# Optimization experiments

Measured on AMD Instinct MI355X. Metric: run time of the kernel, lower is better.

The kernel has to match this reference:

```python
import math
import jax, jax.numpy as jnp
import numpy as np

IN_CH = 512
OUT_CH = 512
KERNEL = 3
STYLE_DIM = 512
B, H, W = 16, 64, 64


def setup_inputs() -> dict:
    key = jax.random.key(0)
    k1, k2, k3, k4 = jax.random.split(key, 4)
    x = jax.random.normal(k1, (B, IN_CH, H, W), dtype=jnp.float32)
    style = jax.random.normal(k2, (B, STYLE_DIM), dtype=jnp.float32)
    # learned params
    weight = jax.random.normal(k3, (1, OUT_CH, IN_CH, KERNEL, KERNEL), dtype=jnp.float32)
    mod_w = jax.random.normal(k4, (IN_CH, STYLE_DIM), dtype=jnp.float32)  # EqualLinear weight (lr_mul=1)
    mod_b = jnp.zeros((IN_CH,), dtype=jnp.float32)
    return {"x": x, "style": style, "weight": weight, "mod_w": mod_w, "mod_b": mod_b}


def reference(x, style, weight, mod_w, mod_b):
    b, c, h, w = x.shape
    lin_scale = 1.0 / math.sqrt(STYLE_DIM)          # EqualLinear scale (lr_mul=1)
    conv_scale = 1.0 / math.sqrt(IN_CH * KERNEL ** 2)
    pad = KERNEL // 2

    # style modulation: (B, in_ch)
    s = style @ (mod_w * lin_scale).T + mod_b
    # modulated per-sample weights: (B, out, in, k, k)
    wmod = conv_scale * weight * s[:, None, :, None, None]
    # demodulation
    d = jax.lax.rsqrt(jnp.sum(wmod ** 2, axis=(2, 3, 4)) + 1e-8)  # (B, out)
    wmod = wmod * d[:, :, None, None, None]

    # grouped conv trick: groups = B
    w_g = wmod.reshape(b * OUT_CH, c, KERNEL, KERNEL)
    x_g = x.reshape(1, b * c, h, w)
    out = jax.lax.conv_general_dilated(
        x_g, w_g,
        window_strides=(1, 1),
        padding=[(pad, pad), (pad, pad)],
        dimension_numbers=("NCHW", "OIHW", "NCHW"),
        feature_group_count=b,
    )
    return out.reshape(b, OUT_CH, out.shape[2], out.shape[3])
```

## Files before the change

### kernel.cpp

```cpp
#include <hip/hip_runtime.h>
#include <hip/hip_bf16.h>
#include <math.h>

typedef __attribute__((ext_vector_type(8))) short short8;
typedef __attribute__((ext_vector_type(4))) float f32x4;

#define BATCH 16
#define IC 512
#define OC 512
#define HW 64
#define SD 512

#define LIN_SCALE 0.04419417382415922f
#define CONV_SCALE 0.014731391274719742f
#define CS2 (1.0f / 4608.0f)

__global__ void k_style(const float* __restrict__ style, const float* __restrict__ mod_w,
                        const float* __restrict__ mod_b, float* __restrict__ s) {
    int idx = blockIdx.x * blockDim.x + threadIdx.x;
    if (idx >= BATCH * IC) return;
    int b = idx / IC, c = idx % IC;
    const float4* st = (const float4*)(style + (size_t)b * SD);
    const float4* mw = (const float4*)(mod_w + (size_t)c * SD);
    float acc = 0.f;
#pragma unroll 4
    for (int k = 0; k < SD / 4; ++k) {
        float4 a = st[k], w = mw[k];
        acc += a.x * w.x + a.y * w.y + a.z * w.z + a.w * w.w;
    }
    s[idx] = acc * LIN_SCALE + mod_b[c];
}

__global__ void k_wsq(const float* __restrict__ weight, float* __restrict__ wsq) {
    int idx = blockIdx.x * blockDim.x + threadIdx.x;
    if (idx >= OC * IC) return;
    const float* w = weight + (size_t)idx * 9;
    float acc = 0.f;
#pragma unroll
    for (int k = 0; k < 9; ++k) { float v = w[k]; acc += v * v; }
    wsq[idx] = acc;
}

__global__ void k_demod(const float* __restrict__ s, const float* __restrict__ wsq,
                        float* __restrict__ dmod) {
    int idx = blockIdx.x * blockDim.x + threadIdx.x;
    if (idx >= BATCH * OC) return;
    int b = idx / OC, o = idx % OC;
    const float* sb = s + (size_t)b * IC;
    const float* wo = wsq + (size_t)o * IC;
    float acc = 0.f;
#pragma unroll 4
    for (int c = 0; c < IC; ++c) { float sv = sb[c]; acc = fmaf(sv * sv, wo[c], acc); }
    dmod[idx] = rsqrtf(acc * CS2 + 1e-8f);
}

__global__ __launch_bounds__(256) void k_wmod(
    const float* __restrict__ weight, const float* __restrict__ s,
    const float* __restrict__ dmod, __hip_bfloat16* __restrict__ wmod) {
    __shared__ float wrow[IC * 9];
    int oc = blockIdx.x, b = blockIdx.y;
    const float* wp = weight + (size_t)oc * IC * 9;
    for (int i = threadIdx.x; i < IC * 9; i += 256) wrow[i] = wp[i];
    __syncthreads();
    float dd = CONV_SCALE * dmod[b * OC + oc];
    const float* sb = s + (size_t)b * IC;
#pragma unroll
    for (int tap = 0; tap < 9; ++tap) {
        int icp = threadIdx.x;
        int ic0 = icp * 2;
        float v0 = wrow[ic0 * 9 + tap] * (sb[ic0] * dd);
        float v1 = wrow[(ic0 + 1) * 9 + tap] * (sb[ic0 + 1] * dd);
        __hip_bfloat162 p;
        p.x = __float2bfloat16(v0);
        p.y = __float2bfloat16(v1);
        *(__hip_bfloat162*)(wmod + ((((size_t)b * 9 + tap) * OC + oc) * IC + ic0)) = p;
    }
}

__global__ __launch_bounds__(512, 2) void k_conv_mfma(
    const float* __restrict__ x, const __hip_bfloat16* __restrict__ wmod,
    float* __restrict__ out) {
    __shared__ short xs[4 * 10 * 66 * 8];

    const int bid = blockIdx.x;
    const int g = bid & 63, sp = bid >> 6;
    const int b = g >> 2, ocg = g & 3;
    const int ocb = ocg * 128, y0 = sp * 8;

    const int t = threadIdx.x;
    const int lane = t & 63, wid = t >> 6;
    const int og = wid >> 2, rg = wid & 3;
    const int l15 = lane & 15, l4 = lane >> 4;

    f32x4 acc[4][8];
#pragma unroll
    for (int m = 0; m < 4; ++m)
#pragma unroll
        for (int n = 0; n < 8; ++n) acc[m][n] = (f32x4){0.f, 0.f, 0.f, 0.f};

    const float* xb = x + (size_t)b * IC * HW * HW;
    const __hip_bfloat16* wb = wmod + (size_t)b * 9 * OC * IC;

    for (int icb = 0; icb < IC; icb += 32) {
        __syncthreads();
        for (int i = t; i < 2640; i += 512) {
            int ichi = i / 660;
            int rem = i - ichi * 660;
            int row = rem / 66;
            int col = rem - row * 66;
            int gy = y0 + row - 1, gx = col - 1;
            float v[8];
            if ((unsigned)gy < 64u && (unsigned)gx < 64u) {
                const float* xp = xb + ((size_t)(icb + ichi * 8) * 64 + gy) * 64 + gx;
#pragma unroll
                for (int j = 0; j < 8; ++j) v[j] = xp[(size_t)j * 4096];
            } else {
#pragma unroll
                for (int j = 0; j < 8; ++j) v[j] = 0.f;
            }
            short8 pk;
#pragma unroll
            for (int j = 0; j < 8; ++j) {
                __hip_bfloat16 bh = __float2bfloat16(v[j]);
                pk[j] = *reinterpret_cast<short*>(&bh);
            }
            *(short8*)&xs[i * 8] = pk;
        }
        __syncthreads();

#pragma unroll
        for (int kw = 0; kw < 3; ++kw) {
            short8 A[3][4];
#pragma unroll
            for (int kh = 0; kh < 3; ++kh)
#pragma unroll
                for (int mt = 0; mt < 4; ++mt) {
                    int oc = ocb + og * 64 + mt * 16 + l15;
                    int tap = kh * 3 + kw;
                    A[kh][mt] = *(const short8*)(wb + (((size_t)tap * OC + oc) * IC + icb + l4 * 8));
                }
#pragma unroll
            for (int cg = 0; cg < 4; ++cg) {
                short8 Bf[4];
#pragma unroll
                for (int ir = 0; ir < 4; ++ir) {
                    int row = rg * 2 + ir;
                    int col = cg * 16 + l15 + kw;
                    Bf[ir] = *(const short8*)&xs[(((l4 * 10 + row) * 66 + col)) * 8];
                }
#pragma unroll
                for (int kh = 0; kh < 3; ++kh)
#pragma unroll
                    for (int mt = 0; mt < 4; ++mt)
#pragma unroll
                        for (int r = 0; r < 2; ++r)
                            acc[mt][r * 4 + cg] = __builtin_amdgcn_mfma_f32_16x16x32_bf16(
                                A[kh][mt], Bf[r + kh], acc[mt][r * 4 + cg], 0, 0, 0);
            }
        }
    }

#pragma unroll
    for (int mt = 0; mt < 4; ++mt)
#pragma unroll
        for (int r = 0; r < 2; ++r)
#pragma unroll
            for (int cg = 0; cg < 4; ++cg) {
                f32x4 v = acc[mt][r * 4 + cg];
                int y = y0 + rg * 2 + r;
                int xcol = cg * 16 + l15;
#pragma unroll
                for (int q = 0; q < 4; ++q) {
                    int oc = ocb + og * 64 + mt * 16 + l4 * 4 + q;
                    out[(((size_t)b * OC + oc) * HW + y) * HW + xcol] = v[q];
                }
            }
}

#define OC_TILE 16
#define ROWS 4
#define ICCH 8
#define XW 67

__global__ __launch_bounds__(256) void k_conv_f32(
    const float* __restrict__ x, const float* __restrict__ weight,
    const float* __restrict__ s, const float* __restrict__ dmod,
    float* __restrict__ out) {
    __shared__ float x_lds[ICCH][ROWS + 2][XW];
    __shared__ float w_lds[OC_TILE][ICCH][9];

    const int b = blockIdx.z;
    const int ocb = blockIdx.y * OC_TILE;
    const int y0 = blockIdx.x * ROWS;

    const int t = threadIdx.x;
    const int gg = t & 63;
    const int ocg = t >> 6;
    const int row = gg >> 4;
    const int col = (gg & 15) * 4;

    float acc[4][4];
#pragma unroll
    for (int j = 0; j < 4; ++j)
#pragma unroll
        for (int i = 0; i < 4; ++i) acc[j][i] = 0.f;

    const float* xb = x + (size_t)b * IC * HW * HW;
    const float* sb = s + (size_t)b * IC;
    const float* db = dmod + (size_t)b * OC;

    for (int icb = 0; icb < IC; icb += ICCH) {
        for (int i = t; i < ICCH * 6 * 66; i += 256) {
            int ic = i / (6 * 66);
            int rem = i - ic * (6 * 66);
            int r = rem / 66;
            int cx = rem - r * 66;
            int gy = y0 + r - 1;
            int gx = cx - 1;
            float v = 0.f;
            if ((unsigned)gy < 64u && (unsigned)gx < 64u)
                v = xb[((size_t)(icb + ic) * 64 + gy) * 64 + gx];
            x_lds[ic][r][cx] = v;
        }
        for (int i = t; i < OC_TILE * ICCH * 9; i += 256) {
            int oc = i / (ICCH * 9);
            int rem = i - oc * (ICCH * 9);
            int ic = rem / 9;
            int kk = rem - ic * 9;
            float sc = CONV_SCALE * sb[icb + ic] * db[ocb + oc];
            w_lds[oc][ic][kk] = weight[((size_t)(ocb + oc) * IC + (icb + ic)) * 9 + kk] * sc;
        }
        __syncthreads();
#pragma unroll
        for (int ic = 0; ic < ICCH; ++ic)
#pragma unroll
            for (int kh = 0; kh < 3; ++kh) {
                float xv[6];
#pragma unroll
                for (int u = 0; u < 6; ++u) xv[u] = x_lds[ic][row + kh][col + u];
#pragma unroll
                for (int kw = 0; kw < 3; ++kw)
#pragma unroll
                    for (int j = 0; j < 4; ++j) {
                        float wv = w_lds[ocg * 4 + j][ic][kh * 3 + kw];
#pragma unroll
                        for (int i2 = 0; i2 < 4; ++i2)
                            acc[j][i2] = fmaf(wv, xv[i2 + kw], acc[j][i2]);
                    }
            }
        __syncthreads();
    }
#pragma unroll
    for (int j = 0; j < 4; ++j) {
        int oc = ocb + ocg * 4 + j;
        float4 v = make_float4(acc[j][0], acc[j][1], acc[j][2], acc[j][3]);
        *(float4*)(out + (((size_t)b * OC + oc) * HW + (y0 + row)) * HW + col) = v;
    }
}

extern "C" void kernel_launch(void* const* d_in, const int* in_sizes, int n_in,
                              void* d_out, int out_size, void* d_ws, size_t ws_size,
                              hipStream_t stream) {
    const float* x      = (const float*)d_in[0];
    const float* style  = (const float*)d_in[1];
    const float* weight = (const float*)d_in[2];
    const float* mod_w  = (const float*)d_in[3];
    const float* mod_b  = (const float*)d_in[4];
    float* out = (float*)d_out;

    float* s    = (float*)d_ws;
    float* wsq  = s + BATCH * IC;
    float* dmod = wsq + (size_t)OC * IC;
    __hip_bfloat16* wmod = (__hip_bfloat16*)(dmod + BATCH * OC);

    const size_t need = (size_t)(BATCH * IC + OC * IC + BATCH * OC) * 4 +
                        (size_t)BATCH * 9 * OC * IC * 2;

    k_style<<<(BATCH * IC + 255) / 256, 256, 0, stream>>>(style, mod_w, mod_b, s);
    k_wsq<<<(OC * IC + 255) / 256, 256, 0, stream>>>(weight, wsq);
    k_demod<<<(BATCH * OC + 255) / 256, 256, 0, stream>>>(s, wsq, dmod);

    if (ws_size >= need) {
        dim3 wg(OC, BATCH);
        k_wmod<<<wg, 256, 0, stream>>>(weight, s, dmod, wmod);
        k_conv_mfma<<<512, 512, 0, stream>>>(x, wmod, out);
    } else {
        dim3 grid(HW / ROWS, OC / OC_TILE, BATCH);
        k_conv_f32<<<grid, 256, 0, stream>>>(x, weight, s, dmod, out);
    }
}
```

Before: 686.3 us.

## Pre-transpose input to padded bf16 NHWC and double-buffer LDS via direct loads

Adds a pre-pass that converts x into a zero-padded channels-last bf16 buffer. The conv kernel can then stage tiles with global_load_lds into double-buffered LDS, with no bounds checks or per-element fp32-to-bf16 conversion in the hot loop. The modulated weights are written in a fragment-friendly tiled layout so A-operand loads become contiguous. This costs an extra workspace buffer and an extra pass over x, and the new path only runs if the workspace is large enough.

```diff
diff --git a/kernel.cpp b/kernel.cpp
--- a/kernel.cpp
+++ b/kernel.cpp
@@ -3,6 +3,7 @@
 #include <math.h>
 
 typedef __attribute__((ext_vector_type(8))) short short8;
+typedef __attribute__((ext_vector_type(4))) short short4v;
 typedef __attribute__((ext_vector_type(4))) float f32x4;
 
 #define BATCH 16
@@ -54,6 +55,172 @@
     dmod[idx] = rsqrtf(acc * CS2 + 1e-8f);
 }
 
+__global__ __launch_bounds__(256) void k_xt(const float* __restrict__ x,
+                                            __hip_bfloat16* __restrict__ xt) {
+    const int r = blockIdx.x, b = blockIdx.y;
+    __hip_bfloat16* dst = xt + ((size_t)b * 66 + r) * 66 * 512;
+    const int t = threadIdx.x;
+
+    if (r == 0 || r == 65) {
+        short4v z = {0, 0, 0, 0};
+        for (int i = t; i < 66 * 512 / 4; i += 256) ((short4v*)dst)[i] = z;
+        return;
+    }
+    __shared__ __hip_bfloat16 tile[64][264];
+    const int y = r - 1;
+    const float* xb = x + (size_t)b * IC * HW * HW + (size_t)y * 64;
+    const int w = t >> 6, l = t & 63;
+
+    for (int h = 0; h < 2; ++h) {
+        for (int k = 0; k < 16; ++k) {
+            int ic = k * 16 + (t >> 4);
+            int px = (t & 15) * 4;
+            float4 v = *(const float4*)(xb + (size_t)(h * 256 + ic) * 4096 + px);
+            tile[px][ic]     = __float2bfloat16(v.x);
+            tile[px + 1][ic] = __float2bfloat16(v.y);
+            tile[px + 2][ic] = __float2bfloat16(v.z);
+            tile[px + 3][ic] = __float2bfloat16(v.w);
+        }
+        __syncthreads();
+        short4v z = {0, 0, 0, 0};
+        for (int c = w; c < 66; c += 4) {
+            short4v val;
+            if (c == 0 || c == 65) val = z;
+            else val = *(const short4v*)&tile[c - 1][l * 4];
+            *(short4v*)(dst + (size_t)c * 512 + h * 256 + l * 4) = val;
+        }
+        __syncthreads();
+    }
+}
+
+__global__ __launch_bounds__(256) void k_wmod2(
+    const float* __restrict__ weight, const float* __restrict__ s,
+    const float* __restrict__ dmod, __hip_bfloat16* __restrict__ wm) {
+    __shared__ float wrow[IC * 9];
+    const int oc = blockIdx.x;
+    const float* wp = weight + (size_t)oc * IC * 9;
+    for (int i = threadIdx.x; i < IC * 9; i += 256) wrow[i] = wp[i];
+    __syncthreads();
+    const int ocf = oc >> 4, ol = oc & 15;
+    const int icp = threadIdx.x, ic0 = icp * 2;
+    const int icc = ic0 >> 5, l4p = (ic0 >> 3) & 3, j = ic0 & 7;
+
+    for (int b = 0; b < BATCH; ++b) {
+        float dd = CONV_SCALE * dmod[b * OC + oc];
+        float2 sv = *(const float2*)(s + (size_t)b * IC + ic0);
+        float m0 = sv.x * dd, m1 = sv.y * dd;
+#pragma unroll
+        for (int tap = 0; tap < 9; ++tap) {
+            float v0 = wrow[ic0 * 9 + tap] * m0;
+            float v1 = wrow[(ic0 + 1) * 9 + tap] * m1;
+            __hip_bfloat162 p;
+            p.x = __float2bfloat16(v0);
+            p.y = __float2bfloat16(v1);
+            size_t off = (((((size_t)(b * 9 + tap) * 32 + ocf) * 16 + icc) * 16 + ol) * 4 + l4p) * 8 + j;
+            *(__hip_bfloat162*)(wm + off) = p;
+        }
+    }
+}
+
+__global__ __launch_bounds__(512, 2) void k_conv_mfma2(
+    const __hip_bfloat16* __restrict__ xt, const __hip_bfloat16* __restrict__ wm,
+    float* __restrict__ out) {
+    __shared__ short xs[2][2640 * 8];
+
+    const int bid = blockIdx.x;
+    const int g = bid & 63, sp = bid >> 6;
+    const int b = g >> 2, ocg = g & 3;
+    const int ocb128 = ocg * 8;
+    const int y0 = sp * 8;
+
+    const int t = threadIdx.x;
+    const int lane = t & 63, wid = t >> 6;
+    const int og = wid >> 2, rg = wid & 3;
+    const int l15 = lane & 15, l4 = lane >> 4;
+
+    const __hip_bfloat16* xtb = xt + (size_t)b * 66 * 66 * 512;
+    const __hip_bfloat16* wb = wm + (size_t)b * 9 * OC * IC;
+
+    f32x4 acc[4][8];
+#pragma unroll
+    for (int m = 0; m < 4; ++m)
+#pragma unroll
+        for (int n = 0; n < 8; ++n) acc[m][n] = (f32x4){0.f, 0.f, 0.f, 0.f};
+
+    auto stage = [&](int buf, int icb) {
+        for (int i = t; i < 2640; i += 512) {
+            int ichi = i / 660;
+            int rem = i - ichi * 660;
+            int row = rem / 66;
+            int col = rem - row * 66;
+            const __hip_bfloat16* src =
+                xtb + ((size_t)((y0 + row) * 66 + col) * 512 + icb + ichi * 8);
+            __builtin_amdgcn_global_load_lds(
+                (const __attribute__((address_space(1))) unsigned int*)src,
+                (__attribute__((address_space(3))) unsigned int*)&xs[buf][i * 8], 16, 0, 0);
+        }
+    };
+
+    stage(0, 0);
+    asm volatile("s_waitcnt vmcnt(0)" ::: "memory");
+    __syncthreads();
+
+    for (int c = 0; c < 16; ++c) {
+        const int buf = c & 1;
+        if (c < 15) stage(buf ^ 1, (c + 1) * 32);
+
+#pragma unroll
+        for (int kw = 0; kw < 3; ++kw) {
+            short8 A[3][4];
+#pragma unroll
+            for (int kh = 0; kh < 3; ++kh)
+#pragma unroll
+                for (int mt = 0; mt < 4; ++mt) {
+                    int tap = kh * 3 + kw;
+                    int ocf = ocb128 + og * 4 + mt;
+                    A[kh][mt] = *(const short8*)(wb +
+                        (((size_t)(tap * 32 + ocf) * 16 + c) * 512 + l15 * 32 + l4 * 8));
+                }
+#pragma unroll
+            for (int cg = 0; cg < 4; ++cg) {
+                short8 Bf[4];
+#pragma unroll
+                for (int ir = 0; ir < 4; ++ir) {
+                    int row = rg * 2 + ir;
+                    int col = cg * 16 + l15 + kw;
+                    Bf[ir] = *(const short8*)&xs[buf][(l4 * 660 + row * 66 + col) * 8];
+                }
+#pragma unroll
+                for (int kh = 0; kh < 3; ++kh)
+#pragma unroll
+                    for (int mt = 0; mt < 4; ++mt)
+#pragma unroll
+                        for (int r = 0; r < 2; ++r)
+                            acc[mt][r * 4 + cg] = __builtin_amdgcn_mfma_f32_16x16x32_bf16(
+                                A[kh][mt], Bf[r + kh], acc[mt][r * 4 + cg], 0, 0, 0);
+            }
+        }
+        asm volatile("s_waitcnt vmcnt(0)" ::: "memory");
+        __syncthreads();
+    }
+
+#pragma unroll
+    for (int mt = 0; mt < 4; ++mt)
+#pragma unroll
+        for (int r = 0; r < 2; ++r)
+#pragma unroll
+            for (int cg = 0; cg < 4; ++cg) {
+                f32x4 v = acc[mt][r * 4 + cg];
+                int y = y0 + rg * 2 + r;
+                int xcol = cg * 16 + l15;
+#pragma unroll
+                for (int q = 0; q < 4; ++q) {
+                    int oc = ocg * 128 + og * 64 + mt * 16 + l4 * 4 + q;
+                    out[(((size_t)b * OC + oc) * HW + y) * HW + xcol] = v[q];
+                }
+            }
+}
+
 __global__ __launch_bounds__(256) void k_wmod(
     const float* __restrict__ weight, const float* __restrict__ s,
     const float* __restrict__ dmod, __hip_bfloat16* __restrict__ wmod) {
@@ -66,8 +233,7 @@
     const float* sb = s + (size_t)b * IC;
 #pragma unroll
     for (int tap = 0; tap < 9; ++tap) {
-        int icp = threadIdx.x;
-        int ic0 = icp * 2;
+        int ic0 = threadIdx.x * 2;
         float v0 = wrow[ic0 * 9 + tap] * (sb[ic0] * dd);
         float v1 = wrow[(ic0 + 1) * 9 + tap] * (sb[ic0 + 1] * dd);
         __hip_bfloat162 p;
@@ -81,26 +247,21 @@
     const float* __restrict__ x, const __hip_bfloat16* __restrict__ wmod,
     float* __restrict__ out) {
     __shared__ short xs[4 * 10 * 66 * 8];
-
     const int bid = blockIdx.x;
     const int g = bid & 63, sp = bid >> 6;
     const int b = g >> 2, ocg = g & 3;
     const int ocb = ocg * 128, y0 = sp * 8;
-
     const int t = threadIdx.x;
     const int lane = t & 63, wid = t >> 6;
     const int og = wid >> 2, rg = wid & 3;
     const int l15 = lane & 15, l4 = lane >> 4;
-
     f32x4 acc[4][8];
 #pragma unroll
     for (int m = 0; m < 4; ++m)
 #pragma unroll
         for (int n = 0; n < 8; ++n) acc[m][n] = (f32x4){0.f, 0.f, 0.f, 0.f};
-
     const float* xb = x + (size_t)b * IC * HW * HW;
     const __hip_bfloat16* wb = wmod + (size_t)b * 9 * OC * IC;
-
     for (int icb = 0; icb < IC; icb += 32) {
         __syncthreads();
         for (int i = t; i < 2640; i += 512) {
@@ -127,7 +288,6 @@
             *(short8*)&xs[i * 8] = pk;
         }
         __syncthreads();
-
 #pragma unroll
         for (int kw = 0; kw < 3; ++kw) {
             short8 A[3][4];
@@ -159,7 +319,6 @@
             }
         }
     }
-
 #pragma unroll
     for (int mt = 0; mt < 4; ++mt)
 #pragma unroll
@@ -181,34 +340,28 @@
 #define ROWS 4
 #define ICCH 8
 #define XW 67
-
 __global__ __launch_bounds__(256) void k_conv_f32(
     const float* __restrict__ x, const float* __restrict__ weight,
     const float* __restrict__ s, const float* __restrict__ dmod,
     float* __restrict__ out) {
     __shared__ float x_lds[ICCH][ROWS + 2][XW];
     __shared__ float w_lds[OC_TILE][ICCH][9];
-
     const int b = blockIdx.z;
     const int ocb = blockIdx.y * OC_TILE;
     const int y0 = blockIdx.x * ROWS;
-
     const int t = threadIdx.x;
     const int gg = t & 63;
     const int ocg = t >> 6;
     const int row = gg >> 4;
     const int col = (gg & 15) * 4;
-
     float acc[4][4];
 #pragma unroll
     for (int j = 0; j < 4; ++j)
 #pragma unroll
         for (int i = 0; i < 4; ++i) acc[j][i] = 0.f;
-
     const float* xb = x + (size_t)b * IC * HW * HW;
     const float* sb = s + (size_t)b * IC;
     const float* db = dmod + (size_t)b * OC;
-
     for (int icb = 0; icb < IC; icb += ICCH) {
         for (int i = t; i < ICCH * 6 * 66; i += 256) {
             int ic = i / (6 * 66);
@@ -272,15 +425,21 @@
     float* wsq  = s + BATCH * IC;
     float* dmod = wsq + (size_t)OC * IC;
     __hip_bfloat16* wmod = (__hip_bfloat16*)(dmod + BATCH * OC);
-
-    const size_t need = (size_t)(BATCH * IC + OC * IC + BATCH * OC) * 4 +
-                        (size_t)BATCH * 9 * OC * IC * 2;
+    const size_t base_bytes = (size_t)(BATCH * IC + OC * IC + BATCH * OC) * 4;
+    const size_t wmod_bytes = (size_t)BATCH * 9 * OC * IC * 2;
+    const size_t xt_bytes   = (size_t)BATCH * 66 * 66 * 512 * 2;
+    __hip_bfloat16* xt = (__hip_bfloat16*)((char*)d_ws + base_bytes + wmod_bytes);
 
     k_style<<<(BATCH * IC + 255) / 256, 256, 0, stream>>>(style, mod_w, mod_b, s);
     k_wsq<<<(OC * IC + 255) / 256, 256, 0, stream>>>(weight, wsq);
     k_demod<<<(BATCH * OC + 255) / 256, 256, 0, stream>>>(s, wsq, dmod);
 
-    if (ws_size >= need) {
+    if (ws_size >= base_bytes + wmod_bytes + xt_bytes) {
+        k_wmod2<<<OC, 256, 0, stream>>>(weight, s, dmod, wmod);
+        dim3 xg(66, BATCH);
+        k_xt<<<xg, 256, 0, stream>>>(x, xt);
+        k_conv_mfma2<<<512, 512, 0, stream>>>(xt, wmod, out);
+    } else if (ws_size >= base_bytes + wmod_bytes) {
         dim3 wg(OC, BATCH);
         k_wmod<<<wg, 256, 0, stream>>>(weight, s, dmod, wmod);
         k_conv_mfma<<<512, 512, 0, stream>>>(x, wmod, out);
```

Result: faster. 599.3 us (-12.7%).
